# Kernel optimization log

Measured on AMD Instinct MI355X. Metric: run time of the kernel, lower is better.

The kernel has to match this reference:

```python
import jax, jax.numpy as jnp
import numpy as np
from jax import lax

B, S, H, E, P, K, R = 64, 512, 768, 32, 16, 9, 6
HEADS, C1, C2 = 4, 128, 64
FEAT = 4 * C2 + 1  # e1, e2, e1*e2, context (64 each) + log-distance


def _ln(x, g, b):
    m = x.mean(-1, keepdims=True)
    v = ((x - m) ** 2).mean(-1, keepdims=True)
    return (x - m) * lax.rsqrt(v + 1e-5) * g + b


def _gat(x, adj, W, a_s, a_d, bias, heads, cout, concat):
    # Dense GATConv over a small fully-masked entity graph. adj[b,i,j]=edge j->i (incl. self-loops).
    h = jnp.einsum('bef,fhc->behc', x, W.reshape(x.shape[-1], heads, cout))
    s = jnp.einsum('behc,hc->bhe', h, a_s)  # source-node attention term
    d = jnp.einsum('behc,hc->bhe', h, a_d)  # target-node attention term
    logits = jax.nn.leaky_relu(d[:, :, :, None] + s[:, :, None, :], 0.2)  # [b,h,i,j]
    logits = jnp.where(adj[:, None, :, :], logits, -1e9)
    att = jax.nn.softmax(logits, axis=-1)
    out = jnp.einsum('bhij,bjhc->bihc', att, h)
    out = out.reshape(out.shape[0], out.shape[1], heads * cout) if concat else out.mean(2)
    return out + bias


def _crf_nll(em, tags, mask, start, end, trans):
    # torchcrf: loss = -mean log-likelihood. em [B,S,K]; tags [B,S]; mask [B,S] bool.
    emt = jnp.transpose(em, (1, 0, 2))
    tgt = tags.T
    mkt = mask.T.astype(em.dtype)
    num0 = start[tgt[0]] + jnp.take_along_axis(emt[0], tgt[0][:, None], 1)[:, 0]

    def nstep(c, inp):
        ptag, sc = c
        e, t, m = inp
        step = trans[ptag, t] + jnp.take_along_axis(e, t[:, None], 1)[:, 0]
        return (jnp.where(m > 0, t, ptag), sc + step * m), None

    (ltag, num), _ = lax.scan(nstep, (tgt[0], num0), (emt[1:], tgt[1:], mkt[1:]))
    num = num + end[ltag]
    a0 = start[None, :] + emt[0]

    def dstep(a, inp):
        e, m = inp
        nxt = jax.scipy.special.logsumexp(a[:, :, None] + trans[None] + e[:, None, :], axis=1)
        return jnp.where(m[:, None] > 0, nxt, a), None

    aT, _ = lax.scan(dstep, a0, (emt[1:], mkt[1:]))
    Z = jax.scipy.special.logsumexp(aT + end[None], axis=1)
    return jnp.mean(Z - num)


def setup_inputs() -> dict:
    key = jax.random.key(0)
    ks = jax.random.split(key, 24)
    n = lambda i, shape, s=0.05: jax.random.normal(ks[i], shape, jnp.float32) * s
    return {
        'sequence_output': jax.random.normal(ks[0], (B, S, H), jnp.float32),
        'attention_mask': jnp.ones((B, S), jnp.int32),
        'ner_labels': jax.random.randint(ks[1], (B, S), 0, K),
        'entity_start': jax.random.randint(ks[2], (B, E), 0, S - 8),
        'entity_len': jax.random.randint(ks[3], (B, E), 0, 8),
        'pair_e1': jax.random.randint(ks[4], (B, P), 0, E),
        'pair_e2': jax.random.randint(ks[5], (B, P), 0, E),
        'pair_labels': jax.random.randint(ks[6], (B, P), 0, 2),
        'adj_mask': jnp.ones((B, E, E), bool),
        'w_ner1': n(7, (H, 256)), 'b_ner1': jnp.zeros((256,), jnp.float32),
        'w_ner2': n(8, (256, K)), 'b_ner2': jnp.zeros((K,), jnp.float32),
        'crf_start': n(9, (K,), 0.1), 'crf_end': n(10, (K,), 0.1), 'crf_trans': n(11, (K, K), 0.1),
        'w_gat1': n(12, (H, HEADS * C1)), 'a_src1': n(13, (HEADS, C1)), 'a_dst1': n(14, (HEADS, C1)),
        'b_gat1': jnp.zeros((HEADS * C1,), jnp.float32),
        'w_gat2': n(15, (HEADS * C1, C2)), 'a_src2': n(16, (1, C2)), 'a_dst2': n(17, (1, C2)),
        'b_gat2': jnp.zeros((C2,), jnp.float32),
        'w_fe': n(18, (FEAT, 512)), 'b_fe': jnp.zeros((512,), jnp.float32),
        'g_fe': jnp.ones((512,), jnp.float32), 'be_fe': jnp.zeros((512,), jnp.float32),
        'w_rc1': n(19, (R, 512, 256)), 'b_rc1': jnp.zeros((R, 256), jnp.float32),
        'g_rc': jnp.ones((R, 256), jnp.float32), 'be_rc': jnp.zeros((R, 256), jnp.float32),
        'w_rc2': n(20, (R, 256, 1)), 'b_rc2': jnp.zeros((R,), jnp.float32),
    }


def reference(sequence_output, attention_mask, ner_labels, entity_start, entity_len,
              pair_e1, pair_e2, pair_labels, adj_mask,
              w_ner1, b_ner1, w_ner2, b_ner2, crf_start, crf_end, crf_trans,
              w_gat1, a_src1, a_dst1, b_gat1, w_gat2, a_src2, a_dst2, b_gat2,
              w_fe, b_fe, g_fe, be_fe, w_rc1, b_rc1, g_rc, be_rc, w_rc2, b_rc2):
    # NER head (dropout off / eval)
    ner_logits = jnp.maximum(sequence_output @ w_ner1 + b_ner1, 0.0) @ w_ner2 + b_ner2
    ner_loss = _crf_nll(ner_logits, ner_labels, attention_mask.astype(bool),
                        crf_start, crf_end, crf_trans)
    # entity span mean-pool via inclusive cumsum trick
    cs = jnp.concatenate([jnp.zeros((B, 1, H), sequence_output.dtype),
                          jnp.cumsum(sequence_output, axis=1)], axis=1)
    e_end = jnp.clip(entity_start + entity_len, 0, S - 1)
    seg = (jnp.take_along_axis(cs, (e_end + 1)[:, :, None], 1)
           - jnp.take_along_axis(cs, entity_start[:, :, None], 1))
    ent = seg / (e_end - entity_start + 1).astype(sequence_output.dtype)[:, :, None]  # [B,E,H]
    x = _gat(ent, adj_mask, w_gat1, a_src1, a_dst1, b_gat1, HEADS, C1, True)
    x = jnp.maximum(x, 0.0)
    x = _gat(x, adj_mask, w_gat2, a_src2, a_dst2, b_gat2, 1, C2, False)  # [B,E,64]
    x1 = jnp.take_along_axis(x, pair_e1[:, :, None], 1)
    x2 = jnp.take_along_axis(x, pair_e2[:, :, None], 1)
    ctx = jnp.broadcast_to(x.mean(1, keepdims=True), (B, P, C2))
    dist = jnp.log(jnp.abs(pair_e1 - pair_e2).astype(x.dtype) + 1.0)[:, :, None]
    pf = jnp.concatenate([x1, x2, x1 * x2, ctx, dist], axis=-1)  # [B,P,257]
    fe = jax.nn.leaky_relu(_ln(pf @ w_fe + b_fe, g_fe, be_fe), 0.01)
    h1 = jnp.einsum('bpf,rfo->rbpo', fe, w_rc1) + b_rc1[:, None, None, :]
    h1 = jax.nn.leaky_relu(_ln(h1, g_rc[:, None, None, :], be_rc[:, None, None, :]), 0.01)
    z = jnp.einsum('rbpo,ro->rbp', h1, w_rc2[:, :, 0]) + b_rc2[:, None, None]
    y = pair_labels.astype(z.dtype)[None]
    # BCEWithLogitsLoss(pos_weight=2.0), mean per relation type, summed over types
    bce = -(2.0 * y * jax.nn.log_sigmoid(z) + (1.0 - y) * jax.nn.log_sigmoid(-z))
    rel_loss = bce.mean(axis=(1, 2)).sum()
    total = ner_loss + rel_loss
    return ner_logits, z, total
```

## Files before the change

kernel.cpp:

```cpp
#include <hip/hip_runtime.h>
#include <math.h>


#define NB 64
#define NS 512
#define NH 768
#define NE 32
#define NP 16
#define NK 9
#define NR 6
#define NHEADS 4
#define NC1 128
#define NC2 64

#define ZOFF 294912
#define TOTOFF 301056

#define WS_ENT   0u
#define WS_HG1   1572864u
#define WS_X1    2621440u
#define WS_H2    3670016u
#define WS_X2    3801088u
#define WS_S1    3932160u
#define WS_D1    3940352u
#define WS_S2    3948544u
#define WS_D2    3950592u
#define WS_CTX   3952640u
#define WS_PF    3956736u
#define WS_FE    4222976u
#define WS_CRF   4747264u
#define WS_REL   4747328u
#define WS_W1T   4747392u
#define WS_WRT   0u
#define WS_WFET  393216u

typedef __attribute__((ext_vector_type(8))) short bf16x8;
typedef __attribute__((ext_vector_type(4))) float f32x4;

__device__ __forceinline__ unsigned short f2bf(float x) {
  union { float f; unsigned u; } v; v.f = x;
  unsigned r = v.u + 0x7FFFu + ((v.u >> 16) & 1u);
  return (unsigned short)(r >> 16);
}

__device__ __forceinline__ float logsigf(float x) {
  if (x >= 0.f) return -log1pf(__expf(-x));
  return x - log1pf(__expf(x));
}

__global__ __launch_bounds__(256) void k_w1t(const float* __restrict__ w1,
    unsigned short* __restrict__ w1t) {
  const int k = blockIdx.x, t = threadIdx.x;
  w1t[t * NH + k] = f2bf(w1[k * 256 + t]);
}

__global__ __launch_bounds__(256) void k_wrt(const float* __restrict__ w1,
    unsigned short* __restrict__ wrt) {
  __shared__ unsigned short tr[256 * 72];
  const int r = blockIdx.x >> 3, kt = blockIdx.x & 7;
  const int k0 = kt * 64, t = threadIdx.x;
#pragma unroll
  for (int i = 0; i < 16; i++) {
    const int slot = t + 256 * i;
    const int row = slot >> 6, c4 = slot & 63;
    const float4 f = *reinterpret_cast<const float4*>(
        &w1[((size_t)(r * 512) + k0 + row) * 256 + c4 * 4]);
    tr[(c4 * 4 + 0) * 72 + row] = f2bf(f.x);
    tr[(c4 * 4 + 1) * 72 + row] = f2bf(f.y);
    tr[(c4 * 4 + 2) * 72 + row] = f2bf(f.z);
    tr[(c4 * 4 + 3) * 72 + row] = f2bf(f.w);
  }
  __syncthreads();
#pragma unroll
  for (int i = 0; i < 8; i++) {
    const int slot = t + 256 * i;
    const int col = slot >> 3, q = slot & 7;
    *reinterpret_cast<uint4*>(&wrt[((size_t)(r * 256 + col)) * 512 + k0 + q * 8]) =
        *reinterpret_cast<const uint4*>(&tr[col * 72 + q * 8]);
  }
}

__global__ __launch_bounds__(256) void k_wfet(const float* __restrict__ w,
    unsigned short* __restrict__ wt) {
  __shared__ unsigned short tr[256 * 72];
  const int kt = blockIdx.x % 5, cb = blockIdx.x / 5;
  const int k0 = kt * 64, c0 = cb * 256, t = threadIdx.x;
#pragma unroll
  for (int i = 0; i < 16; i++) {
    const int slot = t + 256 * i;
    const int row = slot >> 6, c4 = slot & 63;
    const int k = k0 + row;
    float4 f = {0.f, 0.f, 0.f, 0.f};
    if (k < 257)
      f = *reinterpret_cast<const float4*>(&w[(size_t)k * 512 + c0 + c4 * 4]);
    tr[(c4 * 4 + 0) * 72 + row] = f2bf(f.x);
    tr[(c4 * 4 + 1) * 72 + row] = f2bf(f.y);
    tr[(c4 * 4 + 2) * 72 + row] = f2bf(f.z);
    tr[(c4 * 4 + 3) * 72 + row] = f2bf(f.w);
  }
  __syncthreads();
#pragma unroll
  for (int i = 0; i < 8; i++) {
    const int slot = t + 256 * i;
    const int col = slot >> 3, q = slot & 7;
    *reinterpret_cast<uint4*>(&wt[((size_t)(c0 + col)) * 320 + k0 + q * 8]) =
        *reinterpret_cast<const uint4*>(&tr[col * 72 + q * 8]);
  }
}

__global__ __launch_bounds__(256) void k_ner(const float* __restrict__ seq,
    const unsigned short* __restrict__ w1t, const float* __restrict__ b1,
    const float* __restrict__ w2, const float* __restrict__ b2,
    float* __restrict__ out) {
  __shared__ unsigned short AsS[64 * 40];
  __shared__ unsigned short BsS[256 * 40];
  __shared__ float zs[64 * 4 * 12];
  const int t = threadIdx.x;
  const int tok0 = blockIdx.x * 64;
  const int w = t >> 6, lane = t & 63, quad = lane >> 4, l15 = lane & 15;

  f32x4 acc[4][4];
#pragma unroll
  for (int r = 0; r < 4; r++)
#pragma unroll
    for (int c = 0; c < 4; c++) acc[r][c] = (f32x4){0.f, 0.f, 0.f, 0.f};

  const int tokA = t >> 2, koffA = (t & 3) * 8;
  const float* aptr = seq + (size_t)(tok0 + tokA) * NH + koffA;

  for (int kt = 0; kt < NH; kt += 32) {
    __syncthreads();
    {
      const float4 f0 = *reinterpret_cast<const float4*>(aptr + kt);
      const float4 f1 = *reinterpret_cast<const float4*>(aptr + kt + 4);
      bf16x8 av;
      av[0] = (short)f2bf(f0.x); av[1] = (short)f2bf(f0.y);
      av[2] = (short)f2bf(f0.z); av[3] = (short)f2bf(f0.w);
      av[4] = (short)f2bf(f1.x); av[5] = (short)f2bf(f1.y);
      av[6] = (short)f2bf(f1.z); av[7] = (short)f2bf(f1.w);
      *reinterpret_cast<bf16x8*>(&AsS[tokA * 40 + koffA]) = av;
    }
#pragma unroll
    for (int i = 0; i < 4; i++) {
      const int q = t + 256 * i;
      const int col = q >> 2, koff = (q & 3) * 8;
      *reinterpret_cast<uint4*>(&BsS[col * 40 + koff]) =
          *reinterpret_cast<const uint4*>(&w1t[(size_t)col * NH + kt + koff]);
    }
    __syncthreads();
    bf16x8 a[4], b[4];
#pragma unroll
    for (int r = 0; r < 4; r++)
      a[r] = *reinterpret_cast<const bf16x8*>(&AsS[(r * 16 + l15) * 40 + quad * 8]);
#pragma unroll
    for (int c = 0; c < 4; c++)
      b[c] = *reinterpret_cast<const bf16x8*>(&BsS[(w * 64 + c * 16 + l15) * 40 + quad * 8]);
#pragma unroll
    for (int r = 0; r < 4; r++)
#pragma unroll
      for (int c = 0; c < 4; c++)
        acc[r][c] = __builtin_amdgcn_mfma_f32_16x16x32_bf16(a[r], b[c], acc[r][c], 0, 0, 0);
  }

  float b1v[4], w2v[4][NK];
#pragma unroll
  for (int c = 0; c < 4; c++) {
    const int col = w * 64 + c * 16 + l15;
    b1v[c] = b1[col];
#pragma unroll
    for (int cc = 0; cc < NK; cc++) w2v[c][cc] = w2[col * NK + cc];
  }
#pragma unroll
  for (int r = 0; r < 4; r++) {
#pragma unroll
    for (int reg = 0; reg < 4; reg++) {
      float p[NK];
#pragma unroll
      for (int cc = 0; cc < NK; cc++) p[cc] = 0.f;
#pragma unroll
      for (int c = 0; c < 4; c++) {
        const float h = fmaxf(acc[r][c][reg] + b1v[c], 0.f);
#pragma unroll
        for (int cc = 0; cc < NK; cc++) p[cc] = fmaf(h, w2v[c][cc], p[cc]);
      }
#pragma unroll
      for (int o = 1; o < 16; o <<= 1)
#pragma unroll
        for (int cc = 0; cc < NK; cc++) p[cc] += __shfl_xor(p[cc], o);
      if (l15 == 0) {
        const int tokr = r * 16 + quad * 4 + reg;
#pragma unroll
        for (int cc = 0; cc < NK; cc++) zs[(tokr * 4 + w) * 12 + cc] = p[cc];
      }
    }
  }
  __syncthreads();
  if (t < 64) {
#pragma unroll
    for (int cc = 0; cc < NK; cc++) {
      const float z = zs[(t * 4 + 0) * 12 + cc] + zs[(t * 4 + 1) * 12 + cc] +
                      zs[(t * 4 + 2) * 12 + cc] + zs[(t * 4 + 3) * 12 + cc] + b2[cc];
      out[(size_t)(tok0 + t) * NK + cc] = z;
    }
  }
}

__global__ __launch_bounds__(256) void k_crf(const float* __restrict__ em,
    const int* __restrict__ tags, const int* __restrict__ mask,
    const float* __restrict__ startv, const float* __restrict__ endv,
    const float* __restrict__ trans, float* __restrict__ lossb) {
  __shared__ float bufA[64 * 81];
  __shared__ float bufB[32 * 81];
  __shared__ float ems[128 * 9];
  __shared__ int mks[128];
  __shared__ float trs[81];
  __shared__ float qres[4][81];
  __shared__ float av[9];
  __shared__ float red[4];
  const int b = blockIdx.x, t = threadIdx.x;
  const float* emb = em + (size_t)b * NS * NK;
  const int* mk = mask + b * NS;
  const int* tg = tags + b * NS;
  if (t < 81) trs[t] = trans[t];
  if (t < 64) {
    float num = 0.f;
    int lastS = 0;
#pragma unroll
    for (int o = 0; o < 8; o++) {
      const int s = t * 8 + o;
      if (s >= 1 && mk[s] > 0) {
        const int cur = tg[s], prv = tg[s - 1];
        num += trans[prv * NK + cur] + emb[s * NK + cur];
        lastS = s;
      }
    }
#pragma unroll
    for (int o = 32; o > 0; o >>= 1) {
      num += __shfl_xor(num, o);
      lastS = max(lastS, __shfl_xor(lastS, o));
    }
    if (t == 0) {
      const int t0 = tg[0];
      red[0] = startv[t0] + emb[t0] + num + endv[tg[lastS]];
    }
  }

  for (int h = 0; h < 4; h++) {
    const int s0 = 1 + h * 128;
    __syncthreads();
    for (int i = t; i < 128 * 9; i += 256) {
      const int g = s0 * 9 + i;
      ems[i] = (g < NS * 9) ? emb[g] : 0.f;
    }
    if (t < 128) {
      const int s = s0 + t;
      mks[t] = (s < NS) ? mk[s] : 0;
    }
    __syncthreads();
    for (int idx = t; idx < 64 * 81; idx += 256) {
      const int p = idx / 81, e = idx % 81, i = e / 9, j = e % 9;
      const int la = 2 * p, lb = la + 1;
      const bool ma = mks[la] > 0, mb = mks[lb] > 0;
      float r;
      if (ma && mb) {
        float v[9], mx = -1e30f;
#pragma unroll
        for (int m = 0; m < 9; m++) {
          v[m] = trs[i * 9 + m] + ems[la * 9 + m] + trs[m * 9 + j];
          mx = fmaxf(mx, v[m]);
        }
        float sum = 0.f;
#pragma unroll
        for (int m = 0; m < 9; m++) sum += __expf(v[m] - mx);
        r = mx + __logf(sum) + ems[lb * 9 + j];
      } else if (ma) {
        r = trs[e] + ems[la * 9 + j];
      } else if (mb) {
        r = trs[e] + ems[lb * 9 + j];
      } else {
        r = (i == j) ? 0.f : -1e30f;
      }
      bufA[p * 81 + e] = r;
    }
    float* src = bufA;
    float* dst = bufB;
    for (int n = 64; n > 1; n >>= 1) {
      __syncthreads();
      const int half = n >> 1;
      for (int idx = t; idx < half * 81; idx += 256) {
        const int q = idx / 81, e = idx % 81, i = e / 9, j = e % 9;
        const float* A = src + (size_t)(2 * q) * 81;
        const float* Bm = src + (size_t)(2 * q + 1) * 81;
        float v[9], mx = -1e30f;
#pragma unroll
        for (int m = 0; m < 9; m++) {
          v[m] = A[i * 9 + m] + Bm[m * 9 + j];
          mx = fmaxf(mx, v[m]);
        }
        float sum = 0.f;
#pragma unroll
        for (int m = 0; m < 9; m++) sum += __expf(v[m] - mx);
        dst[q * 81 + e] = mx + __logf(sum);
      }
      float* tmp = src; src = dst; dst = tmp;
    }
    __syncthreads();
    if (t < 81) qres[h][t] = src[t];
  }
  __syncthreads();
  if (t < 9) av[t] = startv[t] + emb[t];
  __syncthreads();
  for (int h = 0; h < 4; h++) {
    float nv = 0.f;
    if (t < 9) {
      float v[9], mx = -1e30f;
#pragma unroll
      for (int i2 = 0; i2 < 9; i2++) {
        v[i2] = av[i2] + qres[h][i2 * 9 + t];
        mx = fmaxf(mx, v[i2]);
      }
      float sum = 0.f;
#pragma unroll
      for (int i2 = 0; i2 < 9; i2++) sum += __expf(v[i2] - mx);
      nv = mx + __logf(sum);
    }
    __syncthreads();
    if (t < 9) av[t] = nv;
    __syncthreads();
  }
  if (t == 0) {
    float mx = -1e30f;
#pragma unroll
    for (int j = 0; j < 9; j++) mx = fmaxf(mx, av[j] + endv[j]);
    float sum = 0.f;
#pragma unroll
    for (int j = 0; j < 9; j++) sum += __expf(av[j] + endv[j] - mx);
    lossb[b] = (mx + __logf(sum)) - red[0];
  }
}

__global__ __launch_bounds__(256) void k_ent(const float* __restrict__ seq,
    const int* __restrict__ est, const int* __restrict__ elen, float* __restrict__ ent) {
  const int be = blockIdx.x;
  const int b = be >> 5, e = be & 31;
  const int st = est[b * NE + e];
  int en = st + elen[b * NE + e];
  en = min(max(en, 0), NS - 1);
  const float inv = 1.f / (float)(en - st + 1);
  for (int c = threadIdx.x; c < NH; c += 256) {
    float s = 0.f;
    for (int r = st; r <= en; r++) s += seq[((size_t)b * NS + r) * NH + c];
    ent[((size_t)b * NE + e) * NH + c] = s * inv;
  }
}

__global__ __launch_bounds__(256) void k_g1(const float* __restrict__ ent,
    const float* __restrict__ w, float* __restrict__ hout) {
  __shared__ float As[32 * 36];
  __shared__ float Bs[32 * 128];
  const int b = blockIdx.x >> 2, cb = blockIdx.x & 3;
  const int t = threadIdx.x;
  const int tc = t & 31, tr = t >> 5;
  float acc[4][4];
#pragma unroll
  for (int i = 0; i < 4; i++)
#pragma unroll
    for (int j = 0; j < 4; j++) acc[i][j] = 0.f;
  for (int kt = 0; kt < NH; kt += 32) {
    __syncthreads();
    {
      const int e = t >> 3, k4 = t & 7;
      *reinterpret_cast<float4*>(&As[e * 36 + k4 * 4]) =
          *reinterpret_cast<const float4*>(&ent[((size_t)b * NE + e) * NH + kt + k4 * 4]);
    }
#pragma unroll
    for (int i = 0; i < 4; i++) {
      const int slot = t + 256 * i;
      const int row = slot >> 5, cg = slot & 31;
      *reinterpret_cast<float4*>(&Bs[row * 128 + cg * 4]) =
          *reinterpret_cast<const float4*>(&w[(size_t)(kt + row) * 512 + cb * 128 + cg * 4]);
    }
    __syncthreads();
#pragma unroll
    for (int kg = 0; kg < 8; kg++) {
      float4 a[4];
#pragma unroll
      for (int i = 0; i < 4; i++)
        a[i] = *reinterpret_cast<const float4*>(&As[(tr * 4 + i) * 36 + kg * 4]);
#pragma unroll
      for (int k2 = 0; k2 < 4; k2++) {
        const float4 bv = *reinterpret_cast<const float4*>(&Bs[(kg * 4 + k2) * 128 + tc * 4]);
#pragma unroll
        for (int i = 0; i < 4; i++) {
          const float av = reinterpret_cast<const float*>(&a[i])[k2];
          acc[i][0] = fmaf(av, bv.x, acc[i][0]);
          acc[i][1] = fmaf(av, bv.y, acc[i][1]);
          acc[i][2] = fmaf(av, bv.z, acc[i][2]);
          acc[i][3] = fmaf(av, bv.w, acc[i][3]);
        }
      }
    }
  }
#pragma unroll
  for (int i = 0; i < 4; i++) {
    float4 v;
    v.x = acc[i][0]; v.y = acc[i][1]; v.z = acc[i][2]; v.w = acc[i][3];
    *reinterpret_cast<float4*>(&hout[((size_t)b * NE + tr * 4 + i) * 512 + cb * 128 + tc * 4]) = v;
  }
}

__global__ __launch_bounds__(128) void k_sd1(const float* __restrict__ h,
    const float* __restrict__ as, const float* __restrict__ ad,
    float* __restrict__ s1, float* __restrict__ d1) {
  __shared__ float sm[4];
  const int be = blockIdx.x;
  const int b = be >> 5, e = be & 31;
  const int t = threadIdx.x;
  for (int hd = 0; hd < NHEADS; hd++) {
    const float v = h[((size_t)b * NE + e) * 512 + hd * NC1 + t];
    float sv = v * as[hd * NC1 + t];
    float dv = v * ad[hd * NC1 + t];
#pragma unroll
    for (int o = 32; o > 0; o >>= 1) { sv += __shfl_xor(sv, o); dv += __shfl_xor(dv, o); }
    if ((t & 63) == 0) { sm[(t >> 6) * 2] = sv; sm[(t >> 6) * 2 + 1] = dv; }
    __syncthreads();
    if (t == 0) {
      s1[(b * NHEADS + hd) * NE + e] = sm[0] + sm[2];
      d1[(b * NHEADS + hd) * NE + e] = sm[1] + sm[3];
    }
    __syncthreads();
  }
}

__global__ __launch_bounds__(128) void k_att1(const float* __restrict__ h,
    const float* __restrict__ s1, const float* __restrict__ d1,
    const unsigned char* __restrict__ adj, const float* __restrict__ bias,
    float* __restrict__ x1) {
  __shared__ float att[NE];
  const int blk = blockIdx.x;
  const int i = blk & 31, hd = (blk >> 5) & 3, b = blk >> 7;
  const int t = threadIdx.x;
  if (t < NE) {
    float lg = d1[(b * NHEADS + hd) * NE + i] + s1[(b * NHEADS + hd) * NE + t];
    lg = lg >= 0.f ? lg : 0.2f * lg;
    if (!adj[((size_t)b * NE + i) * NE + t]) lg = -1e9f;
    att[t] = lg;
  }
  __syncthreads();
  if (t == 0) {
    float m = -1e30f;
#pragma unroll
    for (int j = 0; j < NE; j++) m = fmaxf(m, att[j]);
    float ex[NE];
    float sum = 0.f;
#pragma unroll
    for (int j = 0; j < NE; j++) { ex[j] = __expf(att[j] - m); sum += ex[j]; }
    const float inv = 1.f / sum;
#pragma unroll
    for (int j = 0; j < NE; j++) att[j] = ex[j] * inv;
  }
  __syncthreads();
  float acc = bias[hd * NC1 + t];
  for (int j = 0; j < NE; j++)
    acc += att[j] * h[((size_t)b * NE + j) * 512 + hd * NC1 + t];
  x1[((size_t)b * NE + i) * 512 + hd * NC1 + t] = fmaxf(acc, 0.f);
}

__global__ __launch_bounds__(256) void k_g2(const float* __restrict__ x1,
    const float* __restrict__ w, const float* __restrict__ as, const float* __restrict__ ad,
    float* __restrict__ h2, float* __restrict__ s2, float* __restrict__ d2) {
  __shared__ float As[32 * 36];
  __shared__ float Bs[32 * 64];
  const int b = blockIdx.x;
  const int t = threadIdx.x;
  const int tc = t & 15, tr = t >> 4;
  float acc[2][4];
#pragma unroll
  for (int i = 0; i < 2; i++)
#pragma unroll
    for (int j = 0; j < 4; j++) acc[i][j] = 0.f;
  for (int kt = 0; kt < 512; kt += 32) {
    __syncthreads();
    {
      const int e = t >> 3, k4 = t & 7;
      *reinterpret_cast<float4*>(&As[e * 36 + k4 * 4]) =
          *reinterpret_cast<const float4*>(&x1[((size_t)b * NE + e) * 512 + kt + k4 * 4]);
    }
#pragma unroll
    for (int i = 0; i < 2; i++) {
      const int slot = t + 256 * i;
      const int row = slot >> 4, cg = slot & 15;
      *reinterpret_cast<float4*>(&Bs[row * 64 + cg * 4]) =
          *reinterpret_cast<const float4*>(&w[(size_t)(kt + row) * NC2 + cg * 4]);
    }
    __syncthreads();
#pragma unroll
    for (int kg = 0; kg < 8; kg++) {
      float4 a[2];
#pragma unroll
      for (int i = 0; i < 2; i++)
        a[i] = *reinterpret_cast<const float4*>(&As[(tr * 2 + i) * 36 + kg * 4]);
#pragma unroll
      for (int k2 = 0; k2 < 4; k2++) {
        const float4 bv = *reinterpret_cast<const float4*>(&Bs[(kg * 4 + k2) * 64 + tc * 4]);
#pragma unroll
        for (int i = 0; i < 2; i++) {
          const float av = reinterpret_cast<const float*>(&a[i])[k2];
          acc[i][0] = fmaf(av, bv.x, acc[i][0]);
          acc[i][1] = fmaf(av, bv.y, acc[i][1]);
          acc[i][2] = fmaf(av, bv.z, acc[i][2]);
          acc[i][3] = fmaf(av, bv.w, acc[i][3]);
        }
      }
    }
  }
  const float4 a4s = *reinterpret_cast<const float4*>(&as[tc * 4]);
  const float4 a4d = *reinterpret_cast<const float4*>(&ad[tc * 4]);
#pragma unroll
  for (int i = 0; i < 2; i++) {
    const int e = tr * 2 + i;
    float4 v;
    v.x = acc[i][0]; v.y = acc[i][1]; v.z = acc[i][2]; v.w = acc[i][3];
    *reinterpret_cast<float4*>(&h2[((size_t)b * NE + e) * NC2 + tc * 4]) = v;
    float sv = v.x * a4s.x + v.y * a4s.y + v.z * a4s.z + v.w * a4s.w;
    float dv = v.x * a4d.x + v.y * a4d.y + v.z * a4d.z + v.w * a4d.w;
#pragma unroll
    for (int o = 8; o > 0; o >>= 1) { sv += __shfl_xor(sv, o); dv += __shfl_xor(dv, o); }
    if (tc == 0) { s2[b * NE + e] = sv; d2[b * NE + e] = dv; }
  }
}

__global__ __launch_bounds__(64) void k_att2(const float* __restrict__ h2,
    const float* __restrict__ s2, const float* __restrict__ d2,
    const unsigned char* __restrict__ adj, const float* __restrict__ bias,
    float* __restrict__ x2) {
  __shared__ float att[NE];
  const int be = blockIdx.x;
  const int b = be >> 5, i = be & 31;
  const int t = threadIdx.x;
  if (t < NE) {
    float lg = d2[b * NE + i] + s2[b * NE + t];
    lg = lg >= 0.f ? lg : 0.2f * lg;
    if (!adj[((size_t)b * NE + i) * NE + t]) lg = -1e9f;
    att[t] = lg;
  }
  __syncthreads();
  if (t == 0) {
    float m = -1e30f;
#pragma unroll
    for (int j = 0; j < NE; j++) m = fmaxf(m, att[j]);
    float ex[NE];
    float sum = 0.f;
#pragma unroll
    for (int j = 0; j < NE; j++) { ex[j] = __expf(att[j] - m); sum += ex[j]; }
    const float inv = 1.f / sum;
#pragma unroll
    for (int j = 0; j < NE; j++) att[j] = ex[j] * inv;
  }
  __syncthreads();
  float acc = bias[t];
  for (int j = 0; j < NE; j++)
    acc += att[j] * h2[((size_t)b * NE + j) * NC2 + t];
  x2[((size_t)b * NE + i) * NC2 + t] = acc;
}

__global__ __launch_bounds__(64) void k_ctx(const float* __restrict__ x2, float* __restrict__ ctx) {
  const int b = blockIdx.x, t = threadIdx.x;
  float s = 0.f;
  for (int e = 0; e < NE; e++) s += x2[((size_t)b * NE + e) * NC2 + t];
  ctx[b * NC2 + t] = s * (1.f / NE);
}

__global__ __launch_bounds__(64) void k_pf(const float* __restrict__ x2,
    const float* __restrict__ ctx, const int* __restrict__ pe1, const int* __restrict__ pe2,
    float* __restrict__ pf) {
  const int bp = blockIdx.x;
  const int b = bp >> 4, p = bp & 15;
  const int t = threadIdx.x;
  const int e1 = pe1[b * NP + p], e2 = pe2[b * NP + p];
  const float v1 = x2[((size_t)b * NE + e1) * NC2 + t];
  const float v2 = x2[((size_t)b * NE + e2) * NC2 + t];
  float* row = pf + (size_t)bp * 260;
  row[t] = v1;
  row[64 + t] = v2;
  row[128 + t] = v1 * v2;
  row[192 + t] = ctx[b * NC2 + t];
  if (t == 0) row[256] = logf(fabsf((float)(e1 - e2)) + 1.f);
  if (t < 3) row[257 + t] = 0.f;
}

__global__ __launch_bounds__(256) void k_fe(const float* __restrict__ pf,
    const unsigned short* __restrict__ wt, const float* __restrict__ bfe,
    const float* __restrict__ g, const float* __restrict__ be,
    unsigned short* __restrict__ feb) {
  __shared__ unsigned short Af[16 * 320];
  __shared__ float Cs[16 * 520];
  const int b = blockIdx.x, t = threadIdx.x;
  const int w = t >> 6, lane = t & 63, quad = lane >> 4, l15 = lane & 15;
  for (int i = t; i < 16 * 320; i += 256) {
    const int p = i / 320, k = i - p * 320;
    Af[i] = (k < 260) ? f2bf(pf[(size_t)(b * NP + p) * 260 + k]) : (unsigned short)0;
  }
  __syncthreads();
  f32x4 acc[8];
#pragma unroll
  for (int c = 0; c < 8; c++) acc[c] = (f32x4){0.f, 0.f, 0.f, 0.f};
#pragma unroll
  for (int kt = 0; kt < 10; kt++) {
    const bf16x8 a = *reinterpret_cast<const bf16x8*>(&Af[l15 * 320 + kt * 32 + quad * 8]);
#pragma unroll
    for (int c = 0; c < 8; c++) {
      const int col = w * 128 + c * 16 + l15;
      const bf16x8 bv = *reinterpret_cast<const bf16x8*>(&wt[(size_t)col * 320 + kt * 32 + quad * 8]);
      acc[c] = __builtin_amdgcn_mfma_f32_16x16x32_bf16(a, bv, acc[c], 0, 0, 0);
    }
  }
#pragma unroll
  for (int c = 0; c < 8; c++)
#pragma unroll
    for (int reg = 0; reg < 4; reg++)
      Cs[(quad * 4 + reg) * 520 + w * 128 + c * 16 + l15] = acc[c][reg];
  __syncthreads();
  float bfev[8], gv[8], bev[8];
#pragma unroll
  for (int ch = 0; ch < 8; ch++) {
    const int col = ch * 64 + lane;
    bfev[ch] = bfe[col]; gv[ch] = g[col]; bev[ch] = be[col];
  }
#pragma unroll
  for (int pp = 0; pp < 4; pp++) {
    const int p = w * 4 + pp;
    float v[8], s = 0.f, sq = 0.f;
#pragma unroll
    for (int ch = 0; ch < 8; ch++) {
      v[ch] = Cs[p * 520 + ch * 64 + lane] + bfev[ch];
      s += v[ch]; sq += v[ch] * v[ch];
    }
#pragma unroll
    for (int o = 32; o > 0; o >>= 1) { s += __shfl_xor(s, o); sq += __shfl_xor(sq, o); }
    const float mean = s * (1.f / 512.f);
    const float var = sq * (1.f / 512.f) - mean * mean;
    const float rr = rsqrtf(var + 1e-5f);
#pragma unroll
    for (int ch = 0; ch < 8; ch++) {
      float n = (v[ch] - mean) * rr * gv[ch] + bev[ch];
      n = n >= 0.f ? n : 0.01f * n;
      feb[(size_t)(b * NP + p) * 512 + ch * 64 + lane] = f2bf(n);
    }
  }
}

__global__ __launch_bounds__(256) void k_rc(const unsigned short* __restrict__ feb,
    const unsigned short* __restrict__ wrt, const float* __restrict__ b1,
    const float* __restrict__ g, const float* __restrict__ be,
    const float* __restrict__ w2, const float* __restrict__ b2,
    const int* __restrict__ ylab, float* __restrict__ zout, float* __restrict__ relacc) {
  __shared__ unsigned short Af[16 * 520];
  __shared__ float Cs[16 * 264];
  const int blk = blockIdx.x;
  const int r = blk >> 6, b = blk & 63;
  const int t = threadIdx.x;
  const int w = t >> 6, lane = t & 63, quad = lane >> 4, l15 = lane & 15;
#pragma unroll
  for (int i = 0; i < 4; i++) {
    const int slot = t + 256 * i;
    const int p = slot >> 6, q = slot & 63;
    *reinterpret_cast<uint4*>(&Af[p * 520 + q * 8]) =
        *reinterpret_cast<const uint4*>(&feb[(size_t)(b * NP + p) * 512 + q * 8]);
  }
  __syncthreads();
  f32x4 acc[4];
#pragma unroll
  for (int c = 0; c < 4; c++) acc[c] = (f32x4){0.f, 0.f, 0.f, 0.f};
#pragma unroll
  for (int kt = 0; kt < 16; kt++) {
    const bf16x8 a = *reinterpret_cast<const bf16x8*>(&Af[l15 * 520 + kt * 32 + quad * 8]);
#pragma unroll
    for (int c = 0; c < 4; c++) {
      const int col = w * 64 + c * 16 + l15;
      const bf16x8 bv = *reinterpret_cast<const bf16x8*>(
          &wrt[(size_t)(r * 256 + col) * 512 + kt * 32 + quad * 8]);
      acc[c] = __builtin_amdgcn_mfma_f32_16x16x32_bf16(a, bv, acc[c], 0, 0, 0);
    }
  }
#pragma unroll
  for (int c = 0; c < 4; c++)
#pragma unroll
    for (int reg = 0; reg < 4; reg++)
      Cs[(quad * 4 + reg) * 264 + w * 64 + c * 16 + l15] = acc[c][reg];
  __syncthreads();
  float b1v[4], gv[4], bev[4], w2v[4];
#pragma unroll
  for (int ch = 0; ch < 4; ch++) {
    const int col = r * 256 + ch * 64 + lane;
    b1v[ch] = b1[col]; gv[ch] = g[col]; bev[ch] = be[col]; w2v[ch] = w2[col];
  }
  const float b2v = b2[r];
  float local = 0.f;
#pragma unroll
  for (int pp = 0; pp < 4; pp++) {
    const int p = w * 4 + pp;
    float v[4], s = 0.f, sq = 0.f;
#pragma unroll
    for (int ch = 0; ch < 4; ch++) {
      v[ch] = Cs[p * 264 + ch * 64 + lane] + b1v[ch];
      s += v[ch]; sq += v[ch] * v[ch];
    }
#pragma unroll
    for (int o = 32; o > 0; o >>= 1) { s += __shfl_xor(s, o); sq += __shfl_xor(sq, o); }
    const float mean = s * (1.f / 256.f);
    const float var = sq * (1.f / 256.f) - mean * mean;
    const float rr = rsqrtf(var + 1e-5f);
    float zdot = 0.f;
#pragma unroll
    for (int ch = 0; ch < 4; ch++) {
      float n = (v[ch] - mean) * rr * gv[ch] + bev[ch];
      n = n >= 0.f ? n : 0.01f * n;
      zdot = fmaf(n, w2v[ch], zdot);
    }
#pragma unroll
    for (int o = 32; o > 0; o >>= 1) zdot += __shfl_xor(zdot, o);
    if (lane == 0) {
      const float zp = zdot + b2v;
      zout[(size_t)(r * NB + b) * NP + p] = zp;
      const float y = (float)ylab[b * NP + p];
      local += -(2.f * y * logsigf(zp) + (1.f - y) * logsigf(-zp));
    }
  }
  if (lane == 0) atomicAdd(relacc, local * (1.f / (NB * NP)));
}

__global__ __launch_bounds__(64) void k_fin(const float* __restrict__ lossb,
    const float* __restrict__ rel, float* __restrict__ out) {
  float v = lossb[threadIdx.x];
#pragma unroll
  for (int o = 32; o > 0; o >>= 1) v += __shfl_down(v, o);
  if (threadIdx.x == 0) out[TOTOFF] = v * (1.f / NB) + rel[0];
}

extern "C" void kernel_launch(void* const* d_in, const int* in_sizes, int n_in,
                              void* d_out, int out_size, void* d_ws, size_t ws_size,
                              hipStream_t stream) {
  const float* seq = (const float*)d_in[0];
  const int* amask = (const int*)d_in[1];
  const int* nlab = (const int*)d_in[2];
  const int* est = (const int*)d_in[3];
  const int* elen = (const int*)d_in[4];
  const int* pe1 = (const int*)d_in[5];
  const int* pe2 = (const int*)d_in[6];
  const int* plab = (const int*)d_in[7];
  const unsigned char* adj = (const unsigned char*)d_in[8];
  const float* w_ner1 = (const float*)d_in[9];
  const float* b_ner1 = (const float*)d_in[10];
  const float* w_ner2 = (const float*)d_in[11];
  const float* b_ner2 = (const float*)d_in[12];
  const float* crf_start = (const float*)d_in[13];
  const float* crf_end = (const float*)d_in[14];
  const float* crf_trans = (const float*)d_in[15];
  const float* w_gat1 = (const float*)d_in[16];
  const float* a_src1 = (const float*)d_in[17];
  const float* a_dst1 = (const float*)d_in[18];
  const float* b_gat1 = (const float*)d_in[19];
  const float* w_gat2 = (const float*)d_in[20];
  const float* a_src2 = (const float*)d_in[21];
  const float* a_dst2 = (const float*)d_in[22];
  const float* b_gat2 = (const float*)d_in[23];
  const float* w_fe = (const float*)d_in[24];
  const float* b_fe = (const float*)d_in[25];
  const float* g_fe = (const float*)d_in[26];
  const float* be_fe = (const float*)d_in[27];
  const float* w_rc1 = (const float*)d_in[28];
  const float* b_rc1 = (const float*)d_in[29];
  const float* g_rc = (const float*)d_in[30];
  const float* be_rc = (const float*)d_in[31];
  const float* w_rc2 = (const float*)d_in[32];
  const float* b_rc2 = (const float*)d_in[33];

  float* out = (float*)d_out;
  float* ws = (float*)d_ws;
  float* ent = ws + WS_ENT;
  float* hg1 = ws + WS_HG1;
  float* x1 = ws + WS_X1;
  float* h2 = ws + WS_H2;
  float* x2 = ws + WS_X2;
  float* s1 = ws + WS_S1;
  float* d1 = ws + WS_D1;
  float* s2 = ws + WS_S2;
  float* d2 = ws + WS_D2;
  float* ctx = ws + WS_CTX;
  float* pf = ws + WS_PF;
  float* crfb = ws + WS_CRF;
  float* rel = ws + WS_REL;
  unsigned short* w1t = (unsigned short*)(ws + WS_W1T);
  unsigned short* feb = (unsigned short*)(ws + WS_FE);
  unsigned short* wrt = (unsigned short*)(ws + WS_WRT);
  unsigned short* wfet = (unsigned short*)(ws + WS_WFET);

  hipMemsetAsync(rel, 0, sizeof(float), stream);

  k_w1t<<<NH, 256, 0, stream>>>(w_ner1, w1t);
  k_ner<<<512, 256, 0, stream>>>(seq, w1t, b_ner1, w_ner2, b_ner2, out);
  k_crf<<<64, 256, 0, stream>>>(out, nlab, amask, crf_start, crf_end, crf_trans, crfb);
  k_ent<<<NB * NE, 256, 0, stream>>>(seq, est, elen, ent);
  k_g1<<<NB * 4, 256, 0, stream>>>(ent, w_gat1, hg1);
  k_wrt<<<NR * 8, 256, 0, stream>>>(w_rc1, wrt);
  k_wfet<<<10, 256, 0, stream>>>(w_fe, wfet);
  k_sd1<<<NB * NE, 128, 0, stream>>>(hg1, a_src1, a_dst1, s1, d1);
  k_att1<<<NB * NHEADS * NE, 128, 0, stream>>>(hg1, s1, d1, adj, b_gat1, x1);
  k_g2<<<NB, 256, 0, stream>>>(x1, w_gat2, a_src2, a_dst2, h2, s2, d2);
  k_att2<<<NB * NE, 64, 0, stream>>>(h2, s2, d2, adj, b_gat2, x2);
  k_ctx<<<NB, 64, 0, stream>>>(x2, ctx);
  k_pf<<<NB * NP, 64, 0, stream>>>(x2, ctx, pe1, pe2, pf);
  k_fe<<<NB, 256, 0, stream>>>(pf, wfet, b_fe, g_fe, be_fe, feb);
  k_rc<<<NR * NB, 256, 0, stream>>>(feb, wrt, b_rc1, g_rc, be_rc, w_rc2, b_rc2,
                                    plab, out + ZOFF, rel);
  k_fin<<<1, 64, 0, stream>>>(crfb, rel, out);
}
```

Before: 490.0 us.

## Split CRF partition reduction into per-segment kernel and a final fold kernel

```diff
diff --git a/kernel.cpp b/kernel.cpp
--- a/kernel.cpp
+++ b/kernel.cpp
@@ -12,6 +12,8 @@
 #define NHEADS 4
 #define NC1 128
 #define NC2 64
+#define SEGS 16
+#define SEGLEN 32
 
 #define ZOFF 294912
 #define TOTOFF 301056
@@ -33,6 +35,7 @@
 #define WS_W1T   4747392u
 #define WS_WRT   0u
 #define WS_WFET  393216u
+#define WS_SEG   475136u
 
 typedef __attribute__((ext_vector_type(8))) short bf16x8;
 typedef __attribute__((ext_vector_type(4))) float f32x4;
@@ -205,24 +208,95 @@
   }
 }
 
-__global__ __launch_bounds__(256) void k_crf(const float* __restrict__ em,
+__global__ __launch_bounds__(128) void k_crf_seg(const float* __restrict__ em,
+    const int* __restrict__ mask, const float* __restrict__ trans,
+    float* __restrict__ segm) {
+  __shared__ float bufA[16 * 81];
+  __shared__ float bufB[8 * 81];
+  __shared__ float ems[SEGLEN * 9];
+  __shared__ int mks[SEGLEN];
+  __shared__ float trs[81];
+  const int blk = blockIdx.x;
+  const int b = blk >> 4, seg = blk & 15;
+  const int t = threadIdx.x;
+  const int s0 = 1 + seg * SEGLEN;
+  const float* emb = em + (size_t)b * NS * NK;
+  const int* mk = mask + b * NS;
+  if (t < 81) trs[t] = trans[t];
+  for (int i = t; i < SEGLEN * 9; i += 128) {
+    const int g = s0 * 9 + i;
+    ems[i] = (g < NS * 9) ? emb[g] : 0.f;
+  }
+  if (t < SEGLEN) {
+    const int s = s0 + t;
+    mks[t] = (s < NS) ? mk[s] : 0;
+  }
+  __syncthreads();
+  for (int idx = t; idx < 16 * 81; idx += 128) {
+    const int p = idx / 81, e = idx % 81, i = e / 9, j = e % 9;
+    const int la = 2 * p, lb = la + 1;
+    const bool ma = mks[la] > 0, mb = mks[lb] > 0;
+    float r;
+    if (ma && mb) {
+      float v[9], mx = -1e30f;
+#pragma unroll
+      for (int m = 0; m < 9; m++) {
+        v[m] = trs[i * 9 + m] + ems[la * 9 + m] + trs[m * 9 + j];
+        mx = fmaxf(mx, v[m]);
+      }
+      float sum = 0.f;
+#pragma unroll
+      for (int m = 0; m < 9; m++) sum += __expf(v[m] - mx);
+      r = mx + __logf(sum) + ems[lb * 9 + j];
+    } else if (ma) {
+      r = trs[e] + ems[la * 9 + j];
+    } else if (mb) {
+      r = trs[e] + ems[lb * 9 + j];
+    } else {
+      r = (i == j) ? 0.f : -1e30f;
+    }
+    bufA[p * 81 + e] = r;
+  }
+  float* src = bufA;
+  float* dst = bufB;
+  for (int n = 16; n > 1; n >>= 1) {
+    __syncthreads();
+    const int half = n >> 1;
+    for (int idx = t; idx < half * 81; idx += 128) {
+      const int q = idx / 81, e = idx % 81, i = e / 9, j = e % 9;
+      const float* A = src + (size_t)(2 * q) * 81;
+      const float* Bm = src + (size_t)(2 * q + 1) * 81;
+      float v[9], mx = -1e30f;
+#pragma unroll
+      for (int m = 0; m < 9; m++) {
+        v[m] = A[i * 9 + m] + Bm[m * 9 + j];
+        mx = fmaxf(mx, v[m]);
+      }
+      float sum = 0.f;
+#pragma unroll
+      for (int m = 0; m < 9; m++) sum += __expf(v[m] - mx);
+      dst[q * 81 + e] = mx + __logf(sum);
+    }
+    float* tmp = src; src = dst; dst = tmp;
+  }
+  __syncthreads();
+  if (t < 81) segm[((size_t)b * SEGS + seg) * 81 + t] = src[t];
+}
+
+__global__ __launch_bounds__(64) void k_crf_fin(const float* __restrict__ em,
     const int* __restrict__ tags, const int* __restrict__ mask,
     const float* __restrict__ startv, const float* __restrict__ endv,
-    const float* __restrict__ trans, float* __restrict__ lossb) {
-  __shared__ float bufA[64 * 81];
-  __shared__ float bufB[32 * 81];
-  __shared__ float ems[128 * 9];
-  __shared__ int mks[128];
-  __shared__ float trs[81];
-  __shared__ float qres[4][81];
-  __shared__ float av[9];
-  __shared__ float red[4];
+    const float* __restrict__ trans, const float* __restrict__ segm,
+    float* __restrict__ lossb) {
+  __shared__ float sm[SEGS * 81];
+  __shared__ float av[16];
+  __shared__ float red[2];
   const int b = blockIdx.x, t = threadIdx.x;
   const float* emb = em + (size_t)b * NS * NK;
   const int* mk = mask + b * NS;
   const int* tg = tags + b * NS;
-  if (t < 81) trs[t] = trans[t];
-  if (t < 64) {
+  for (int i = t; i < SEGS * 81; i += 64) sm[i] = segm[(size_t)b * SEGS * 81 + i];
+  {
     float num = 0.f;
     int lastS = 0;
 #pragma unroll
@@ -244,79 +318,16 @@
       red[0] = startv[t0] + emb[t0] + num + endv[tg[lastS]];
     }
   }
-
-  for (int h = 0; h < 4; h++) {
-    const int s0 = 1 + h * 128;
-    __syncthreads();
-    for (int i = t; i < 128 * 9; i += 256) {
-      const int g = s0 * 9 + i;
-      ems[i] = (g < NS * 9) ? emb[g] : 0.f;
-    }
-    if (t < 128) {
-      const int s = s0 + t;
-      mks[t] = (s < NS) ? mk[s] : 0;
-    }
-    __syncthreads();
-    for (int idx = t; idx < 64 * 81; idx += 256) {
-      const int p = idx / 81, e = idx % 81, i = e / 9, j = e % 9;
-      const int la = 2 * p, lb = la + 1;
-      const bool ma = mks[la] > 0, mb = mks[lb] > 0;
-      float r;
-      if (ma && mb) {
-        float v[9], mx = -1e30f;
-#pragma unroll
-        for (int m = 0; m < 9; m++) {
-          v[m] = trs[i * 9 + m] + ems[la * 9 + m] + trs[m * 9 + j];
-          mx = fmaxf(mx, v[m]);
-        }
-        float sum = 0.f;
-#pragma unroll
-        for (int m = 0; m < 9; m++) sum += __expf(v[m] - mx);
-        r = mx + __logf(sum) + ems[lb * 9 + j];
-      } else if (ma) {
-        r = trs[e] + ems[la * 9 + j];
-      } else if (mb) {
-        r = trs[e] + ems[lb * 9 + j];
-      } else {
-        r = (i == j) ? 0.f : -1e30f;
-      }
-      bufA[p * 81 + e] = r;
-    }
-    float* src = bufA;
-    float* dst = bufB;
-    for (int n = 64; n > 1; n >>= 1) {
-      __syncthreads();
-      const int half = n >> 1;
-      for (int idx = t; idx < half * 81; idx += 256) {
-        const int q = idx / 81, e = idx % 81, i = e / 9, j = e % 9;
-        const float* A = src + (size_t)(2 * q) * 81;
-        const float* Bm = src + (size_t)(2 * q + 1) * 81;
-        float v[9], mx = -1e30f;
-#pragma unroll
-        for (int m = 0; m < 9; m++) {
-          v[m] = A[i * 9 + m] + Bm[m * 9 + j];
-          mx = fmaxf(mx, v[m]);
-        }
-        float sum = 0.f;
-#pragma unroll
-        for (int m = 0; m < 9; m++) sum += __expf(v[m] - mx);
-        dst[q * 81 + e] = mx + __logf(sum);
-      }
-      float* tmp = src; src = dst; dst = tmp;
-    }
-    __syncthreads();
-    if (t < 81) qres[h][t] = src[t];
-  }
   __syncthreads();
   if (t < 9) av[t] = startv[t] + emb[t];
   __syncthreads();
-  for (int h = 0; h < 4; h++) {
+  for (int h = 0; h < SEGS; h++) {
     float nv = 0.f;
     if (t < 9) {
       float v[9], mx = -1e30f;
 #pragma unroll
       for (int i2 = 0; i2 < 9; i2++) {
-        v[i2] = av[i2] + qres[h][i2 * 9 + t];
+        v[i2] = av[i2] + sm[h * 81 + i2 * 9 + t];
         mx = fmaxf(mx, v[i2]);
       }
       float sum = 0.f;
@@ -795,16 +806,19 @@
   unsigned short* feb = (unsigned short*)(ws + WS_FE);
   unsigned short* wrt = (unsigned short*)(ws + WS_WRT);
   unsigned short* wfet = (unsigned short*)(ws + WS_WFET);
+  float* segm = ws + WS_SEG;
 
   hipMemsetAsync(rel, 0, sizeof(float), stream);
 
   k_w1t<<<NH, 256, 0, stream>>>(w_ner1, w1t);
   k_ner<<<512, 256, 0, stream>>>(seq, w1t, b_ner1, w_ner2, b_ner2, out);
-  k_crf<<<64, 256, 0, stream>>>(out, nlab, amask, crf_start, crf_end, crf_trans, crfb);
   k_ent<<<NB * NE, 256, 0, stream>>>(seq, est, elen, ent);
   k_g1<<<NB * 4, 256, 0, stream>>>(ent, w_gat1, hg1);
   k_wrt<<<NR * 8, 256, 0, stream>>>(w_rc1, wrt);
   k_wfet<<<10, 256, 0, stream>>>(w_fe, wfet);
+  k_crf_seg<<<NB * SEGS, 128, 0, stream>>>(out, amask, crf_trans, segm);
+  k_crf_fin<<<NB, 64, 0, stream>>>(out, nlab, amask, crf_start, crf_end, crf_trans,
+                                   segm, crfb);
   k_sd1<<<NB * NE, 128, 0, stream>>>(hg1, a_src1, a_dst1, s1, d1);
   k_att1<<<NB * NHEADS * NE, 128, 0, stream>>>(hg1, s1, d1, adj, b_gat1, x1);
   k_g2<<<NB, 256, 0, stream>>>(x1, w_gat2, a_src2, a_dst2, h2, s2, d2);
```

New measurement: 449.2 us. 1.09x faster.
